# Kernel optimization log

Hardware: AMD Instinct MI355X
Metric: run time of the kernel (lower is better)

## Reference

```python
import jax, jax.numpy as jnp
import numpy as np

H = 512; W = 512; C = 32; E = 32; NH = 2; HD = 16; B = 4; N = 50000
SHIFTS = jnp.array([[0, 0], [-1, 0], [1, 0], [0, 1], [-1, 1], [1, 1], [0, -1], [-1, -1], [1, -1]], dtype=jnp.int32)


def setup_inputs() -> dict:
    key = jax.random.key(0)
    ks = jax.random.split(key, 12)

    def coords(k):
        # unique BEV cells per sample -> well-defined coord->index lookup
        flat = jax.random.permutation(k, H * W)[:N]
        return jnp.stack([flat // W, flat % W], axis=-1).astype(jnp.int32)

    li_coors = jnp.stack([coords(jax.random.fold_in(ks[0], b)) for b in range(B)])
    ra_coors = jnp.stack([coords(jax.random.fold_in(ks[1], b)) for b in range(B)])
    li_feats = jax.random.normal(ks[2], (B, N, C), jnp.float32)
    ra_feats = jax.random.normal(ks[3], (B, N, C), jnp.float32)
    s = 0.1
    return {
        "li_feats": li_feats, "li_coors": li_coors,
        "ra_feats": ra_feats, "ra_coors": ra_coors,
        "w_qkv1": jax.random.normal(ks[4], (3 * E, E), jnp.float32) * s,
        "b_qkv1": jax.random.normal(ks[5], (3 * E,), jnp.float32) * s,
        "w_out1": jax.random.normal(ks[6], (E, E), jnp.float32) * s,
        "b_out1": jax.random.normal(ks[7], (E,), jnp.float32) * s,
        "w_qkv2": jax.random.normal(ks[8], (3 * E, E), jnp.float32) * s,
        "b_qkv2": jax.random.normal(ks[9], (3 * E,), jnp.float32) * s,
        "w_out2": jax.random.normal(ks[10], (E, E), jnp.float32) * s,
        "b_out2": jax.random.normal(ks[11], (E,), jnp.float32) * s,
    }


def _mha(q, kv, w_qkv, b_qkv, w_out, b_out):
    # q: [N,1,E], kv: [N,9,E]; torch MultiheadAttention (eval, dropout off)
    wq, wk, wv = jnp.split(w_qkv, 3, axis=0)
    bq, bk, bv = jnp.split(b_qkv, 3)
    n = q.shape[0]
    Q = (q @ wq.T + bq).reshape(n, 1, NH, HD)
    K = (kv @ wk.T + bk).reshape(n, 9, NH, HD)
    V = (kv @ wv.T + bv).reshape(n, 9, NH, HD)
    s = jnp.einsum('nqhd,nkhd->nhqk', Q, K) / jnp.sqrt(jnp.float32(HD))
    a = jax.nn.softmax(s, axis=-1)
    o = jnp.einsum('nhqk,nkhd->nqhd', a, V).reshape(n, E)
    return o @ w_out.T + b_out


def _gather_keys(q_coor, kv_coor, kv_feat):
    # dense grid lookup: BEV cell -> voxel index in kv (-1 if empty)
    nk = kv_coor.shape[0]
    grid = jnp.full((H * W,), -1, jnp.int32).at[kv_coor[:, 0] * W + kv_coor[:, 1]].set(
        jnp.arange(nk, dtype=jnp.int32))
    sh = q_coor[:, None, :] + SHIFTS[None]  # [N,9,2]
    valid = (sh[..., 0] >= 0) & (sh[..., 0] < H) & (sh[..., 1] >= 0) & (sh[..., 1] < W)
    flat = jnp.clip(sh[..., 0], 0, H - 1) * W + jnp.clip(sh[..., 1], 0, W - 1)
    idx = jnp.where(valid, grid[flat], -1)  # [N,9]
    keys = jnp.where((idx >= 0)[..., None], kv_feat[jnp.clip(idx, 0)], 0.0)
    return keys  # [N,9,C]


def _scatter(feat, coor):
    # PointPillarsScatter: place [N,C] voxel feats into dense [C,H,W] canvas
    flat = coor[:, 0] * W + coor[:, 1]
    return jnp.zeros((C, H * W), feat.dtype).at[:, flat].set(feat.T).reshape(C, H, W)


def _branch(q_feat, q_coor, kv_feat, kv_coor, w_qkv, b_qkv, w_out, b_out):
    keys = _gather_keys(q_coor, kv_coor, kv_feat)
    out = _mha(q_feat[:, None, :], keys, w_qkv, b_qkv, w_out, b_out)
    return _scatter(q_feat + out, q_coor)


def reference(li_feats, li_coors, ra_feats, ra_coors,
              w_qkv1, b_qkv1, w_out1, b_out1,
              w_qkv2, b_qkv2, w_out2, b_out2):
    vb = jax.vmap(_branch, in_axes=(0, 0, 0, 0, None, None, None, None))
    li_img = vb(li_feats, li_coors, ra_feats, ra_coors, w_qkv1, b_qkv1, w_out1, b_out1)
    ra_img = vb(ra_feats, ra_coors, li_feats, li_coors, w_qkv2, b_qkv2, w_out2, b_out2)
    return (li_img, ra_img)  # each [B, C, H, W]
```

## Files before the change

kernel.cpp:

```cpp
#include <hip/hip_runtime.h>

#define HH 512
#define WW 512
#define HWC (HH * WW)
#define NV 50000
#define NB 4
#define NR (NB * NV)
#define NQ (2 * NR)
#define KVROWS (NR + 1)

typedef unsigned int uint32;

static __device__ __forceinline__ float4 ld4(const float* p) {
    return *reinterpret_cast<const float4*>(p);
}
static __device__ __forceinline__ uint32 bf16rne(float x) {
    uint32 u = __float_as_uint(x);
    return (u + 0x7FFFu + ((u >> 16) & 1u)) >> 16;
}
template <int CTRL>
static __device__ __forceinline__ float dpp_add(float x) {
    float t = __int_as_float(__builtin_amdgcn_update_dpp(0, __float_as_int(x), CTRL, 0xF, 0xF, true));
    return x + t;
}

__global__ void k_fill(int4* __restrict__ p) {
    const int total = 2 * NB * HWC / 4;
    const int stride = gridDim.x * blockDim.x;
    const int4 v = make_int4(-1, -1, -1, -1);
    for (int i = blockIdx.x * blockDim.x + threadIdx.x; i < total; i += stride)
        p[i] = v;
}

__global__ void k_grid(const int* __restrict__ li_coors, const int* __restrict__ ra_coors,
                       int* __restrict__ grids) {
    int t = blockIdx.x * blockDim.x + threadIdx.x;
    if (t >= NQ) return;
    int set = t / NR;
    int r2 = t - set * NR;
    int b = r2 / NV;
    int n = r2 - b * NV;
    const int* co = (set == 0 ? li_coors : ra_coors) + (size_t)(b * NV + n) * 2;
    grids[(set * NB + b) * HWC + co[0] * WW + co[1]] = n;
}

__launch_bounds__(256)
__global__ void k_proj_kv(const float* __restrict__ li_feats, const float* __restrict__ ra_feats,
                          const float* __restrict__ w_qkv1, const float* __restrict__ b_qkv1,
                          const float* __restrict__ w_qkv2, const float* __restrict__ b_qkv2,
                          uint32* __restrict__ KV) {
    const int f = blockIdx.y;
    const float* feats = f ? ra_feats : li_feats;
    const float* wkv_g = f ? w_qkv1 : w_qkv2;
    const float* bkv_g = f ? b_qkv1 : b_qkv2;

    __shared__ float xs[4][2][64];
    const int wave = threadIdx.x >> 6;
    const int l    = threadIdx.x & 63;
    const int h    = l >> 5;
    const int j    = l & 31;

    const int gw = blockIdx.x * 4 + wave;
    const int gs = gridDim.x * 4;

    int r0 = gw * 2;
    float xreg = feats[(size_t)r0 * 32 + l];

    float4 wk[8], wv[8];
#pragma unroll
    for (int i = 0; i < 8; ++i) {
        wk[i] = ld4(wkv_g + (32 + j) * 32 + i * 4);
        wv[i] = ld4(wkv_g + (64 + j) * 32 + i * 4);
    }
    const float bk = bkv_g[32 + j], bv = bkv_g[64 + j];

    uint32* KVb = KV + (size_t)(f ^ 1) * KVROWS * 32;

    if (blockIdx.x == 0 && threadIdx.x < 32)
        KVb[(size_t)NR * 32 + threadIdx.x] = bf16rne(bk) | (bf16rne(bv) << 16);

    int cur = 0;
    while (r0 < NR) {
        xs[wave][cur][l] = xreg;
        const int rn = r0 + gs * 2;
        if (rn < NR) xreg = feats[(size_t)rn * 32 + l];

        const float* xp = &xs[wave][cur][h * 32];
        float ak = bk, av = bv;
#pragma unroll
        for (int i = 0; i < 8; ++i) {
            float4 x = *reinterpret_cast<const float4*>(xp + i * 4);
            ak += x.x * wk[i].x + x.y * wk[i].y + x.z * wk[i].z + x.w * wk[i].w;
            av += x.x * wv[i].x + x.y * wv[i].y + x.z * wv[i].z + x.w * wv[i].w;
        }
        KVb[(size_t)(r0 + h) * 32 + j] = bf16rne(ak) | (bf16rne(av) << 16);
        r0 = rn;
        cur ^= 1;
    }
}

__global__ void k_nbr(const int* __restrict__ li_coors, const int* __restrict__ ra_coors,
                      const int* __restrict__ grids, int* __restrict__ nbr) {
    int q = blockIdx.x * 256 + threadIdx.x;
    if (q >= NQ) return;
    int br  = (q >= NR) ? 1 : 0;
    int rem = q - br * NR;
    int b   = rem / NV;
    const int* qc = br ? ra_coors : li_coors;
    const int* kvgrid = grids + ((br ^ 1) * NB + b) * HWC;
    const int2 rc = *reinterpret_cast<const int2*>(qc + (size_t)rem * 2);

    const int drs[9] = {0, -1, 1, 0, -1, 1, 0, -1, 1};
    const int dcs[9] = {0, 0, 0, 1, 1, 1, -1, -1, -1};
    const int base = b * NV;
    int v[9];
#pragma unroll
    for (int k = 0; k < 9; ++k) {
        int rr = rc.x + drs[k], cc = rc.y + dcs[k];
        bool valid = ((unsigned)rr < HH) & ((unsigned)cc < WW);
        int raw = kvgrid[valid ? rr * WW + cc : 0];
        int id = valid ? raw : -1;
        v[k] = (id >= 0 ? base + id : NR) * 128;
    }
    int4* np = reinterpret_cast<int4*>(nbr + (size_t)q * 12);
    np[0] = make_int4(v[0], v[1], v[2], v[3]);
    np[1] = make_int4(v[4], v[5], v[6], v[7]);
    np[2] = make_int4(v[8], 0, 0, 0);
}

__launch_bounds__(256)
__global__ void k_attn(const int* __restrict__ nbr,
                       const float* __restrict__ li_feats, const float* __restrict__ ra_feats,
                       const float* __restrict__ w_qkv1, const float* __restrict__ b_qkv1,
                       const float* __restrict__ w_out1, const float* __restrict__ b_out1,
                       const float* __restrict__ w_qkv2, const float* __restrict__ b_qkv2,
                       const float* __restrict__ w_out2, const float* __restrict__ b_out2,
                       const uint32* __restrict__ KV, float* __restrict__ res) {
    __shared__ float xs[8][4][32];
    __shared__ float Qls[4][8][36];
    __shared__ float os[4][8][36];
    const int tid = threadIdx.x;
    const int w = tid >> 6;
    const int l = tid & 63;
    const int g = tid >> 5;
    const int j = tid & 31;
    const int wq0 = (blockIdx.x * 4 + w) * 8;
    const int br  = (wq0 >= NR) ? 1 : 0;
    const float* feats = br ? ra_feats : li_feats;
    const float* wqkv  = br ? w_qkv2 : w_qkv1;
    const float* bqkv  = br ? b_qkv2 : b_qkv1;
    const float* wout  = br ? w_out2 : w_out1;
    const float* bout  = br ? b_out2 : b_out1;
    const char* KVbr = (const char*)(KV + (size_t)br * KVROWS * 32);

    const int qB = wq0 + (l >> 3);
    const int4* np = reinterpret_cast<const int4*>(nbr + (size_t)qB * 12);
    int4 b0 = np[0], b1 = np[1], b2 = np[2];
    const int coff = (l & 7) * 16;
    int off[9] = {b0.x, b0.y, b0.z, b0.w, b1.x, b1.y, b1.z, b1.w, b2.x};
    uint4 kv4[9];
#pragma unroll
    for (int k = 0; k < 9; ++k)
        kv4[k] = *reinterpret_cast<const uint4*>(KVbr + (size_t)(unsigned)(off[k] + coff));

    const int qrow = (l >> 5) << 2;
    const int remA = wq0 + qrow - br * NR;
    float fr[4];
#pragma unroll
    for (int u = 0; u < 4; ++u) {
        fr[u] = feats[(size_t)(remA + u) * 32 + j];
        xs[g][u][j] = fr[u];
    }
    const float bq = bqkv[j];
    float Qf[4] = {bq, bq, bq, bq};
#pragma unroll
    for (int i = 0; i < 8; ++i) {
        float4 wv4 = ld4(wqkv + j * 32 + i * 4);
#pragma unroll
        for (int u = 0; u < 4; ++u) {
            float4 x = *reinterpret_cast<const float4*>(&xs[g][u][i * 4]);
            Qf[u] += x.x * wv4.x + x.y * wv4.y + x.z * wv4.z + x.w * wv4.w;
        }
    }
    const float SC = 0.25f * 1.44269504f;
#pragma unroll
    for (int u = 0; u < 4; ++u) Qls[w][qrow + u][j] = Qf[u] * SC;

    float4 q4 = *reinterpret_cast<const float4*>(&Qls[w][l >> 3][(l & 7) * 4]);
    float o0 = 0.f, o1 = 0.f, o2 = 0.f, o3 = 0.f, sum = 0.f;
#pragma unroll
    for (int k = 0; k < 9; ++k) {
        uint4 c = kv4[k];
        float k0 = __uint_as_float(c.x << 16);
        float k1 = __uint_as_float(c.y << 16);
        float k2 = __uint_as_float(c.z << 16);
        float k3 = __uint_as_float(c.w << 16);
        float d = q4.x * k0 + q4.y * k1 + q4.z * k2 + q4.w * k3;
        d = dpp_add<0xB1>(d);
        d = dpp_add<0x4E>(d);
        float e = exp2f(d);
        sum += e;
        o0 += e * __uint_as_float(c.x & 0xFFFF0000u);
        o1 += e * __uint_as_float(c.y & 0xFFFF0000u);
        o2 += e * __uint_as_float(c.z & 0xFFFF0000u);
        o3 += e * __uint_as_float(c.w & 0xFFFF0000u);
    }
    const float rs = 1.0f / sum;
    *reinterpret_cast<float4*>(&os[w][l >> 3][(l & 7) * 4]) =
        make_float4(o0 * rs, o1 * rs, o2 * rs, o3 * rs);

    const float bo = bout[j];
    float outv[4] = {bo, bo, bo, bo};
#pragma unroll
    for (int i = 0; i < 8; ++i) {
        float4 wv4 = ld4(wout + j * 32 + i * 4);
#pragma unroll
        for (int u = 0; u < 4; ++u) {
            float4 x = *reinterpret_cast<const float4*>(&os[w][qrow + u][i * 4]);
            outv[u] += x.x * wv4.x + x.y * wv4.y + x.z * wv4.z + x.w * wv4.w;
        }
    }
#pragma unroll
    for (int u = 0; u < 4; ++u)
        res[(size_t)(wq0 + qrow + u) * 32 + j] = fr[u] + outv[u];
}

__launch_bounds__(256)
__global__ void k_densify(const int* __restrict__ grids, const float* __restrict__ res,
                          float* __restrict__ out) {
    int t = blockIdx.x * 256 + threadIdx.x;
    int plane = t >> 18;
    int s = t & (HWC - 1);
    int gidx = grids[t];
    float4 v[8];
    if (gidx >= 0) {
        const float* rp = res + ((size_t)plane * NV + gidx) * 32;
#pragma unroll
        for (int i = 0; i < 8; ++i) v[i] = ld4(rp + i * 4);
    } else {
#pragma unroll
        for (int i = 0; i < 8; ++i) v[i] = make_float4(0.f, 0.f, 0.f, 0.f);
    }
    float* ob = out + (size_t)plane * 32 * HWC + s;
#pragma unroll
    for (int i = 0; i < 8; ++i) {
        __builtin_nontemporal_store(v[i].x, ob + (size_t)(4 * i + 0) * HWC);
        __builtin_nontemporal_store(v[i].y, ob + (size_t)(4 * i + 1) * HWC);
        __builtin_nontemporal_store(v[i].z, ob + (size_t)(4 * i + 2) * HWC);
        __builtin_nontemporal_store(v[i].w, ob + (size_t)(4 * i + 3) * HWC);
    }
}

extern "C" void kernel_launch(void* const* d_in, const int* in_sizes, int n_in,
                              void* d_out, int out_size, void* d_ws, size_t ws_size,
                              hipStream_t stream) {
    const float* li_feats = (const float*)d_in[0];
    const int*   li_coors = (const int*)d_in[1];
    const float* ra_feats = (const float*)d_in[2];
    const int*   ra_coors = (const int*)d_in[3];
    const float* w_qkv1 = (const float*)d_in[4];
    const float* b_qkv1 = (const float*)d_in[5];
    const float* w_out1 = (const float*)d_in[6];
    const float* b_out1 = (const float*)d_in[7];
    const float* w_qkv2 = (const float*)d_in[8];
    const float* b_qkv2 = (const float*)d_in[9];
    const float* w_out2 = (const float*)d_in[10];
    const float* b_out2 = (const float*)d_in[11];
    float* out = (float*)d_out;

    char* ws = (char*)d_ws;
    size_t off = 0;
    int*    grids = (int*)(ws + off);    off += (size_t)2 * NB * HWC * 4;
    uint32* KV    = (uint32*)(ws + off); off += (size_t)2 * KVROWS * 32 * 4;
    float*  res   = (float*)(ws + off);  off += (size_t)NQ * 32 * 4;
    int*    nbr   = (int*)(ws + off);    off += (size_t)NQ * 12 * 4;

    k_fill<<<2048, 256, 0, stream>>>((int4*)grids);

    k_grid<<<(NQ + 255) / 256, 256, 0, stream>>>(li_coors, ra_coors, grids);

    k_proj_kv<<<dim3(3200, 2), 256, 0, stream>>>(
        li_feats, ra_feats, w_qkv1, b_qkv1, w_qkv2, b_qkv2, KV);

    k_nbr<<<(NQ + 255) / 256, 256, 0, stream>>>(li_coors, ra_coors, grids, nbr);

    k_attn<<<NQ / 32, 256, 0, stream>>>(
        nbr, li_feats, ra_feats,
        w_qkv1, b_qkv1, w_out1, b_out1,
        w_qkv2, b_qkv2, w_out2, b_out2,
        KV, res);

    k_densify<<<(2 * NB * HWC) / 256, 256, 0, stream>>>(grids, res, out);
}
```

Measured before the change: 258.0 us.

## Store attention residual in bf16 and use bf16 dot2 for Q and output projections

The attention kernel now keeps the per-voxel result buffer in bf16 instead of fp32, which halves the intermediate written by attention and read back by the densify kernel. The Q and output projections pack weights and activations to bf16 and accumulate with fdot2 instructions, with a fallback path when that builtin is unavailable. The KV projection grid is also doubled. The final output values lose precision through bf16 rounding of the residual sum, which risks tolerance failures.

```diff
diff --git a/kernel.cpp b/kernel.cpp
--- a/kernel.cpp
+++ b/kernel.cpp
@@ -10,6 +10,7 @@
 #define KVROWS (NR + 1)
 
 typedef unsigned int uint32;
+typedef unsigned short ushort16;
 
 static __device__ __forceinline__ float4 ld4(const float* p) {
     return *reinterpret_cast<const float4*>(p);
@@ -17,12 +18,30 @@
 static __device__ __forceinline__ uint32 bf16rne(float x) {
     uint32 u = __float_as_uint(x);
     return (u + 0x7FFFu + ((u >> 16) & 1u)) >> 16;
+}
+static __device__ __forceinline__ uint32 pack2(float a, float b) {
+    return bf16rne(a) | (bf16rne(b) << 16);
 }
 template <int CTRL>
 static __device__ __forceinline__ float dpp_add(float x) {
     float t = __int_as_float(__builtin_amdgcn_update_dpp(0, __float_as_int(x), CTRL, 0xF, 0xF, true));
     return x + t;
 }
+
+typedef short sh2 __attribute__((ext_vector_type(2)));
+#if defined(__has_builtin) && __has_builtin(__builtin_amdgcn_fdot2_f32_bf16)
+static __device__ __forceinline__ float dot2bf(uint32 a, uint32 b, float c) {
+    union U { uint32 u; sh2 v; };
+    U ua; ua.u = a;
+    U ub; ub.u = b;
+    return __builtin_amdgcn_fdot2_f32_bf16(ua.v, ub.v, c, false);
+}
+#else
+static __device__ __forceinline__ float dot2bf(uint32 a, uint32 b, float c) {
+    return fmaf(__uint_as_float(a << 16), __uint_as_float(b << 16),
+           fmaf(__uint_as_float(a & 0xFFFF0000u), __uint_as_float(b & 0xFFFF0000u), c));
+}
+#endif
 
 __global__ void k_fill(int4* __restrict__ p) {
     const int total = 2 * NB * HWC / 4;
@@ -77,7 +96,7 @@
     uint32* KVb = KV + (size_t)(f ^ 1) * KVROWS * 32;
 
     if (blockIdx.x == 0 && threadIdx.x < 32)
-        KVb[(size_t)NR * 32 + threadIdx.x] = bf16rne(bk) | (bf16rne(bv) << 16);
+        KVb[(size_t)NR * 32 + threadIdx.x] = pack2(bk, bv);
 
     int cur = 0;
     while (r0 < NR) {
@@ -93,7 +112,7 @@
             ak += x.x * wk[i].x + x.y * wk[i].y + x.z * wk[i].z + x.w * wk[i].w;
             av += x.x * wv[i].x + x.y * wv[i].y + x.z * wv[i].z + x.w * wv[i].w;
         }
-        KVb[(size_t)(r0 + h) * 32 + j] = bf16rne(ak) | (bf16rne(av) << 16);
+        KVb[(size_t)(r0 + h) * 32 + j] = pack2(ak, av);
         r0 = rn;
         cur ^= 1;
     }
@@ -135,10 +154,10 @@
                        const float* __restrict__ w_out1, const float* __restrict__ b_out1,
                        const float* __restrict__ w_qkv2, const float* __restrict__ b_qkv2,
                        const float* __restrict__ w_out2, const float* __restrict__ b_out2,
-                       const uint32* __restrict__ KV, float* __restrict__ res) {
-    __shared__ float xs[8][4][32];
+                       const uint32* __restrict__ KV, ushort16* __restrict__ resh) {
+    __shared__ ushort16 xsh[8][4][32];
     __shared__ float Qls[4][8][36];
-    __shared__ float os[4][8][36];
+    __shared__ uint32 osu[4][8][20];
     const int tid = threadIdx.x;
     const int w = tid >> 6;
     const int l = tid & 63;
@@ -169,17 +188,26 @@
 #pragma unroll
     for (int u = 0; u < 4; ++u) {
         fr[u] = feats[(size_t)(remA + u) * 32 + j];
-        xs[g][u][j] = fr[u];
+        xsh[g][u][j] = (ushort16)bf16rne(fr[u]);
+    }
+    uint32 wq16[16];
+#pragma unroll
+    for (int i = 0; i < 8; ++i) {
+        float4 wv4 = ld4(wqkv + j * 32 + i * 4);
+        wq16[2 * i]     = pack2(wv4.x, wv4.y);
+        wq16[2 * i + 1] = pack2(wv4.z, wv4.w);
     }
     const float bq = bqkv[j];
     float Qf[4] = {bq, bq, bq, bq};
 #pragma unroll
-    for (int i = 0; i < 8; ++i) {
-        float4 wv4 = ld4(wqkv + j * 32 + i * 4);
+    for (int i = 0; i < 4; ++i) {
 #pragma unroll
         for (int u = 0; u < 4; ++u) {
-            float4 x = *reinterpret_cast<const float4*>(&xs[g][u][i * 4]);
-            Qf[u] += x.x * wv4.x + x.y * wv4.y + x.z * wv4.z + x.w * wv4.w;
+            uint4 x = *reinterpret_cast<const uint4*>(&xsh[g][u][i * 8]);
+            Qf[u] = dot2bf(wq16[i * 4 + 0], x.x, Qf[u]);
+            Qf[u] = dot2bf(wq16[i * 4 + 1], x.y, Qf[u]);
+            Qf[u] = dot2bf(wq16[i * 4 + 2], x.z, Qf[u]);
+            Qf[u] = dot2bf(wq16[i * 4 + 3], x.w, Qf[u]);
         }
     }
     const float SC = 0.25f * 1.44269504f;
@@ -206,48 +234,60 @@
         o3 += e * __uint_as_float(c.w & 0xFFFF0000u);
     }
     const float rs = 1.0f / sum;
-    *reinterpret_cast<float4*>(&os[w][l >> 3][(l & 7) * 4]) =
-        make_float4(o0 * rs, o1 * rs, o2 * rs, o3 * rs);
-
+    *reinterpret_cast<uint2*>(&osu[w][l >> 3][(l & 7) * 2]) =
+        make_uint2(pack2(o0 * rs, o1 * rs), pack2(o2 * rs, o3 * rs));
+
+    uint32 wo16[16];
+#pragma unroll
+    for (int i = 0; i < 8; ++i) {
+        float4 wv4 = ld4(wout + j * 32 + i * 4);
+        wo16[2 * i]     = pack2(wv4.x, wv4.y);
+        wo16[2 * i + 1] = pack2(wv4.z, wv4.w);
+    }
     const float bo = bout[j];
     float outv[4] = {bo, bo, bo, bo};
 #pragma unroll
-    for (int i = 0; i < 8; ++i) {
-        float4 wv4 = ld4(wout + j * 32 + i * 4);
+    for (int i = 0; i < 4; ++i) {
 #pragma unroll
         for (int u = 0; u < 4; ++u) {
-            float4 x = *reinterpret_cast<const float4*>(&os[w][qrow + u][i * 4]);
-            outv[u] += x.x * wv4.x + x.y * wv4.y + x.z * wv4.z + x.w * wv4.w;
+            uint4 x = *reinterpret_cast<const uint4*>(&osu[w][qrow + u][i * 4]);
+            outv[u] = dot2bf(wo16[i * 4 + 0], x.x, outv[u]);
+            outv[u] = dot2bf(wo16[i * 4 + 1], x.y, outv[u]);
+            outv[u] = dot2bf(wo16[i * 4 + 2], x.z, outv[u]);
+            outv[u] = dot2bf(wo16[i * 4 + 3], x.w, outv[u]);
         }
     }
 #pragma unroll
     for (int u = 0; u < 4; ++u)
-        res[(size_t)(wq0 + qrow + u) * 32 + j] = fr[u] + outv[u];
+        resh[(size_t)(wq0 + qrow + u) * 32 + j] = (ushort16)bf16rne(fr[u] + outv[u]);
 }
 
 __launch_bounds__(256)
-__global__ void k_densify(const int* __restrict__ grids, const float* __restrict__ res,
+__global__ void k_densify(const int* __restrict__ grids, const ushort16* __restrict__ resh,
                           float* __restrict__ out) {
     int t = blockIdx.x * 256 + threadIdx.x;
     int plane = t >> 18;
     int s = t & (HWC - 1);
     int gidx = grids[t];
-    float4 v[8];
+    uint4 r[4];
     if (gidx >= 0) {
-        const float* rp = res + ((size_t)plane * NV + gidx) * 32;
-#pragma unroll
-        for (int i = 0; i < 8; ++i) v[i] = ld4(rp + i * 4);
+        const uint4* rp = reinterpret_cast<const uint4*>(resh + (size_t)(plane * (size_t)NV + gidx) * 32);
+#pragma unroll
+        for (int i = 0; i < 4; ++i) r[i] = rp[i];
     } else {
 #pragma unroll
-        for (int i = 0; i < 8; ++i) v[i] = make_float4(0.f, 0.f, 0.f, 0.f);
+        for (int i = 0; i < 4; ++i) r[i] = make_uint4(0, 0, 0, 0);
     }
     float* ob = out + (size_t)plane * 32 * HWC + s;
 #pragma unroll
-    for (int i = 0; i < 8; ++i) {
-        __builtin_nontemporal_store(v[i].x, ob + (size_t)(4 * i + 0) * HWC);
-        __builtin_nontemporal_store(v[i].y, ob + (size_t)(4 * i + 1) * HWC);
-        __builtin_nontemporal_store(v[i].z, ob + (size_t)(4 * i + 2) * HWC);
-        __builtin_nontemporal_store(v[i].w, ob + (size_t)(4 * i + 3) * HWC);
+    for (int i = 0; i < 4; ++i) {
+        uint32 um[4] = {r[i].x, r[i].y, r[i].z, r[i].w};
+#pragma unroll
+        for (int m = 0; m < 4; ++m) {
+            int c = i * 8 + m * 2;
+            __builtin_nontemporal_store(__uint_as_float(um[m] << 16), ob + (size_t)c * HWC);
+            __builtin_nontemporal_store(__uint_as_float(um[m] & 0xFFFF0000u), ob + (size_t)(c + 1) * HWC);
+        }
     }
 }
 
@@ -270,16 +310,16 @@
 
     char* ws = (char*)d_ws;
     size_t off = 0;
-    int*    grids = (int*)(ws + off);    off += (size_t)2 * NB * HWC * 4;
-    uint32* KV    = (uint32*)(ws + off); off += (size_t)2 * KVROWS * 32 * 4;
-    float*  res   = (float*)(ws + off);  off += (size_t)NQ * 32 * 4;
-    int*    nbr   = (int*)(ws + off);    off += (size_t)NQ * 12 * 4;
+    int*      grids = (int*)(ws + off);      off += (size_t)2 * NB * HWC * 4;
+    uint32*   KV    = (uint32*)(ws + off);   off += (size_t)2 * KVROWS * 32 * 4;
+    ushort16* resh  = (ushort16*)(ws + off); off += (size_t)NQ * 32 * 2;
+    int*      nbr   = (int*)(ws + off);      off += (size_t)NQ * 12 * 4;
 
     k_fill<<<2048, 256, 0, stream>>>((int4*)grids);
 
     k_grid<<<(NQ + 255) / 256, 256, 0, stream>>>(li_coors, ra_coors, grids);
 
-    k_proj_kv<<<dim3(3200, 2), 256, 0, stream>>>(
+    k_proj_kv<<<dim3(6400, 2), 256, 0, stream>>>(
         li_feats, ra_feats, w_qkv1, b_qkv1, w_qkv2, b_qkv2, KV);
 
     k_nbr<<<(NQ + 255) / 256, 256, 0, stream>>>(li_coors, ra_coors, grids, nbr);
@@ -288,7 +328,7 @@
         nbr, li_feats, ra_feats,
         w_qkv1, b_qkv1, w_out1, b_out1,
         w_qkv2, b_qkv2, w_out2, b_out2,
-        KV, res);
-
-    k_densify<<<(2 * NB * HWC) / 256, 256, 0, stream>>>(grids, res, out);
-}
+        KV, resh);
+
+    k_densify<<<(2 * NB * HWC) / 256, 256, 0, stream>>>(grids, resh, out);
+}
```

Measured after the change: 294.6 us. +14.2%, slower.
